# Kernel tuning notes

Measured on AMD Instinct MI355X. Metric: run time of the kernel, lower is better.

Reference implementation:

```python
import jax, jax.numpy as jnp
import numpy as np

MANT_BITS = 8  # static quantize_param_dict values for Positional_0/1/2
_PWL_X = jnp.linspace(-4.0, 4.0, 33, dtype=jnp.float32)
_PWL_Y = 0.5 * _PWL_X * (1.0 + jax.lax.erf(_PWL_X / jnp.sqrt(jnp.float32(2.0))))


def float2fix(x, mantissa_bits):
    """Fixed-point quantization: round to multiples of 2^-mantissa_bits (STE grad)."""
    s = jnp.float32(2.0 ** mantissa_bits)
    q = jnp.round(x * s) / s
    return x + jax.lax.stop_gradient(q - x)


def pwlin_gelu_basic(x, mantissa_bits_in, mantissa_bits_out):
    """Piecewise-linear GELU: quantized input, linear interp of exact GELU on
    [-4,4] (33 breakpoints), 0 for x<-4, identity for x>4, quantized output."""
    xq = float2fix(x, mantissa_bits_in)
    y = jnp.interp(xq, _PWL_X, _PWL_Y)
    y = jnp.where(xq > 4.0, xq, jnp.where(xq < -4.0, jnp.float32(0.0), y))
    return float2fix(y, mantissa_bits_out)


def setup_inputs() -> dict:
    key = jax.random.key(0)
    k_x, k_w1, k_b1, k_w2, k_b2 = jax.random.split(key, 5)
    dim, ff_dim = 1024, 4096
    B, S = 32, 512
    sc1 = 1.0 / np.sqrt(dim)
    sc2 = 1.0 / np.sqrt(ff_dim)
    return {
        "x": jax.random.normal(k_x, (B, S, dim), dtype=jnp.float32),
        "w1": jax.random.uniform(k_w1, (dim, ff_dim), jnp.float32, -sc1, sc1),
        "b1": jax.random.uniform(k_b1, (ff_dim,), jnp.float32, -sc1, sc1),
        "w2": jax.random.uniform(k_w2, (ff_dim, dim), jnp.float32, -sc2, sc2),
        "b2": jax.random.uniform(k_b2, (dim,), jnp.float32, -sc2, sc2),
    }


def reference(x, w1, b1, w2, b2):
    # fc1 GEMM + quantize epilogue
    h = jnp.einsum("bsd,df->bsf", x, w1) + b1          # [B,S,ff_dim]
    h = float2fix(h, MANT_BITS)                         # Positional_0
    # piecewise-linear GELU with quantized in/out
    h = pwlin_gelu_basic(h, MANT_BITS, MANT_BITS)
    h = float2fix(h, MANT_BITS)                         # Positional_1
    # fc2 GEMM + quantize epilogue
    out = jnp.einsum("bsf,fd->bsd", h, w2) + b2         # [B,S,dim]
    return float2fix(out, MANT_BITS)                    # Positional_2
```

## Files before the change

kernel.cpp:

```cpp
#include <hip/hip_runtime.h>
#include <hip/hip_bf16.h>

typedef __bf16 bf16_t;
typedef __bf16 bf16x8 __attribute__((ext_vector_type(8)));
typedef __bf16 bf16x4 __attribute__((ext_vector_type(4)));
typedef float f32x4 __attribute__((ext_vector_type(4)));

#define QS   256.0f
#define QINV 0.00390625f

__device__ __forceinline__ void async_copy16(const bf16_t* g, bf16_t* l) {
  __builtin_amdgcn_global_load_lds(
      (__attribute__((address_space(1))) void*)g,
      (__attribute__((address_space(3))) void*)l,
      16, 0, 0);
}

template <bool GELU, typename OutT>
__global__ __launch_bounds__(256, 4)
void gemm_tile(const bf16_t* __restrict__ A, const bf16_t* __restrict__ Bt,
               const float* __restrict__ bias, OutT* __restrict__ C,
               int M, int N, int K) {
  __shared__ __attribute__((aligned(16))) bf16_t As[128 * 64];
  __shared__ __attribute__((aligned(16))) bf16_t Bs[128 * 64];
  __shared__ float Yt[33];

  const int tid = threadIdx.x;
  const int lane = tid & 63;
  const int wv = tid >> 6;
  const int wy = wv >> 1;
  const int wx = wv & 1;
  const int l15 = lane & 15;
  const int lq = lane >> 4;

  if (GELU && tid < 33) {
    float xv = -4.0f + 0.25f * (float)tid;
    Yt[tid] = 0.5f * xv * (1.0f + erff(xv * 0.70710678f));
  }

  const int mBase = blockIdx.y * 128;
  const int nBase = blockIdx.x * 128;

  const bf16_t* aTile = A + (size_t)mBase * K;
  const bf16_t* bTile = Bt + (size_t)nBase * K;

  f32x4 acc[4][4];
#pragma unroll
  for (int i = 0; i < 4; ++i)
#pragma unroll
    for (int j = 0; j < 4; ++j)
      acc[i][j] = (f32x4){0.f, 0.f, 0.f, 0.f};

  const int srow = tid >> 3;
  const int scb = (((tid & 7) ^ ((tid >> 3) & 7)) * 8);

  const int swz_r = l15 & 7;

  for (int k0 = 0; k0 < K; k0 += 64) {
#pragma unroll
    for (int p = 0; p < 4; ++p) {
      const int row = p * 32 + srow;
      const size_t go = (size_t)row * K + k0 + scb;
      const int lo = (p * 256 + wv * 64) * 8;
      async_copy16(aTile + go, As + lo);
      async_copy16(bTile + go, Bs + lo);
    }
    __syncthreads();

#pragma unroll
    for (int ks = 0; ks < 2; ++ks) {
      const int swzA = ((ks * 4 + lq) ^ swz_r) * 8;
      bf16x8 af[4], bfr[4];
#pragma unroll
      for (int i = 0; i < 4; ++i) {
        af[i]  = *(const bf16x8*)(As + (wy * 64 + i * 16 + l15) * 64 + swzA);
        bfr[i] = *(const bf16x8*)(Bs + (wx * 64 + i * 16 + l15) * 64 + swzA);
      }
#pragma unroll
      for (int i = 0; i < 4; ++i)
#pragma unroll
        for (int j = 0; j < 4; ++j)
          acc[i][j] = __builtin_amdgcn_mfma_f32_16x16x32_bf16(af[i], bfr[j], acc[i][j], 0, 0, 0);
    }
    __syncthreads();
  }

  float bj[4];
#pragma unroll
  for (int j = 0; j < 4; ++j)
    bj[j] = bias[nBase + wx * 64 + j * 16 + l15];

#pragma unroll
  for (int i = 0; i < 4; ++i) {
    const int rb = mBase + wy * 64 + i * 16 + lq * 4;
#pragma unroll
    for (int j = 0; j < 4; ++j) {
      const int cn = nBase + wx * 64 + j * 16 + l15;
#pragma unroll
      for (int r = 0; r < 4; ++r) {
        float c = acc[i][j][r] + bj[j];
        float v;
        if (GELU) {
          float xq = rintf(c * QS) * QINV;
          if (xq > 4.0f) {
            v = xq;
          } else if (xq < -4.0f) {
            v = 0.0f;
          } else {
            float t = (xq + 4.0f) * 4.0f;
            int ii = (int)t;
            ii = ii > 31 ? 31 : ii;
            float f = t - (float)ii;
            float y0 = Yt[ii];
            v = fmaf(f, Yt[ii + 1] - y0, y0);
          }
          v = rintf(v * QS) * QINV;
        } else {
          v = rintf(c * QS) * QINV;
        }
        C[(size_t)(rb + r) * N + cn] = (OutT)v;
      }
    }
  }
}

__global__ void cvt_bf16_kernel(const float* __restrict__ in, bf16_t* __restrict__ out, int n4) {
  int idx = blockIdx.x * blockDim.x + threadIdx.x;
  if (idx < n4) {
    const float4 v = ((const float4*)in)[idx];
    bf16x4 o;
    o[0] = (bf16_t)v.x; o[1] = (bf16_t)v.y; o[2] = (bf16_t)v.z; o[3] = (bf16_t)v.w;
    ((bf16x4*)out)[idx] = o;
  }
}

__global__ void transpose_cvt_kernel(const float* __restrict__ in, bf16_t* __restrict__ out,
                                     int R, int C) {
  __shared__ float t[32][33];
  const int c0 = blockIdx.x * 32;
  const int r0 = blockIdx.y * 32;
  const int tx = threadIdx.x;
  const int ty = threadIdx.y;
#pragma unroll
  for (int dy = 0; dy < 32; dy += 8)
    t[ty + dy][tx] = in[(size_t)(r0 + ty + dy) * C + c0 + tx];
  __syncthreads();
#pragma unroll
  for (int dy = 0; dy < 32; dy += 8)
    out[(size_t)(c0 + ty + dy) * R + r0 + tx] = (bf16_t)t[tx][ty + dy];
}

extern "C" void kernel_launch(void* const* d_in, const int* in_sizes, int n_in,
                              void* d_out, int out_size, void* d_ws, size_t ws_size,
                              hipStream_t stream) {
  const float* x  = (const float*)d_in[0];
  const float* w1 = (const float*)d_in[1];
  const float* b1 = (const float*)d_in[2];
  const float* w2 = (const float*)d_in[3];
  const float* b2 = (const float*)d_in[4];
  float* out = (float*)d_out;

  const int M = 16384, D = 1024, F = 4096;

  char* ws = (char*)d_ws;
  size_t off = 0;
  bf16_t* xb  = (bf16_t*)(ws + off); off += (size_t)M * D * 2;
  bf16_t* w1t = (bf16_t*)(ws + off); off += (size_t)D * F * 2;
  bf16_t* w2t = (bf16_t*)(ws + off); off += (size_t)F * D * 2;
  bf16_t* h   = (bf16_t*)(ws + off);

  cvt_bf16_kernel<<<(M * D / 4 + 255) / 256, 256, 0, stream>>>(x, xb, M * D / 4);
  transpose_cvt_kernel<<<dim3(F / 32, D / 32), dim3(32, 8), 0, stream>>>(w1, w1t, D, F);
  transpose_cvt_kernel<<<dim3(D / 32, F / 32), dim3(32, 8), 0, stream>>>(w2, w2t, F, D);

  gemm_tile<true, bf16_t><<<dim3(F / 128, M / 128), 256, 0, stream>>>(xb, w1t, b1, h, M, F, D);
  gemm_tile<false, float><<<dim3(D / 128, M / 128), 256, 0, stream>>>(h, w2t, b2, out, M, D, F);
}
```

Before: 453.5 us.

## Switch GEMMs to 32x32x16 MFMA and remap fc2 blocks per XCD

Replaces the 4x4 grid of 16x16x32 MFMAs per wave with a 2x2 grid of 32x32x16 MFMAs. This halves the number of LDS fragment loads per k-step and uses the larger-tile instruction, and the epilogue indexing is rewritten to match the 32x32 accumulator layout. It also adds a block-index remap for the fc2 GEMM so that blocks landing on the same XCD share A rows, which should improve L2 reuse. The epilogue stores become less contiguous per lane group, and the remap is hardcoded for an 8x128 grid.

```diff
diff --git a/kernel.cpp b/kernel.cpp
--- a/kernel.cpp
+++ b/kernel.cpp
@@ -4,7 +4,7 @@
 typedef __bf16 bf16_t;
 typedef __bf16 bf16x8 __attribute__((ext_vector_type(8)));
 typedef __bf16 bf16x4 __attribute__((ext_vector_type(4)));
-typedef float f32x4 __attribute__((ext_vector_type(4)));
+typedef float f32x16 __attribute__((ext_vector_type(16)));
 
 #define QS   256.0f
 #define QINV 0.00390625f
@@ -16,7 +16,7 @@
       16, 0, 0);
 }
 
-template <bool GELU, typename OutT>
+template <bool GELU, typename OutT, bool XSWZ>
 __global__ __launch_bounds__(256, 4)
 void gemm_tile(const bf16_t* __restrict__ A, const bf16_t* __restrict__ Bt,
                const float* __restrict__ bias, OutT* __restrict__ C,
@@ -30,31 +30,40 @@
   const int wv = tid >> 6;
   const int wy = wv >> 1;
   const int wx = wv & 1;
-  const int l15 = lane & 15;
-  const int lq = lane >> 4;
+  const int l31 = lane & 31;
+  const int hh = lane >> 5;
 
   if (GELU && tid < 33) {
     float xv = -4.0f + 0.25f * (float)tid;
     Yt[tid] = 0.5f * xv * (1.0f + erff(xv * 0.70710678f));
   }
 
-  const int mBase = blockIdx.y * 128;
-  const int nBase = blockIdx.x * 128;
+  int bx = blockIdx.x, by = blockIdx.y;
+  if (XSWZ) {
+    const int f = by * 8 + bx;
+    const int xcd = f & 7;
+    const int s = f >> 3;
+    bx = s & 7;
+    by = xcd * 16 + (s >> 3);
+  }
+
+  const int mBase = by * 128;
+  const int nBase = bx * 128;
 
   const bf16_t* aTile = A + (size_t)mBase * K;
   const bf16_t* bTile = Bt + (size_t)nBase * K;
 
-  f32x4 acc[4][4];
+  f32x16 acc[2][2];
 #pragma unroll
-  for (int i = 0; i < 4; ++i)
+  for (int i = 0; i < 2; ++i)
 #pragma unroll
-    for (int j = 0; j < 4; ++j)
-      acc[i][j] = (f32x4){0.f, 0.f, 0.f, 0.f};
+    for (int j = 0; j < 2; ++j)
+      acc[i][j] = (f32x16){0.f};
 
   const int srow = tid >> 3;
   const int scb = (((tid & 7) ^ ((tid >> 3) & 7)) * 8);
 
-  const int swz_r = l15 & 7;
+  const int swz_r = l31 & 7;
 
   for (int k0 = 0; k0 < K; k0 += 64) {
 #pragma unroll
@@ -68,37 +77,37 @@
     __syncthreads();
 
 #pragma unroll
-    for (int ks = 0; ks < 2; ++ks) {
-      const int swzA = ((ks * 4 + lq) ^ swz_r) * 8;
-      bf16x8 af[4], bfr[4];
+    for (int ks = 0; ks < 4; ++ks) {
+      const int chunk = ((ks * 2 + hh) ^ swz_r) * 8;
+      bf16x8 af[2], bfr[2];
 #pragma unroll
-      for (int i = 0; i < 4; ++i) {
-        af[i]  = *(const bf16x8*)(As + (wy * 64 + i * 16 + l15) * 64 + swzA);
-        bfr[i] = *(const bf16x8*)(Bs + (wx * 64 + i * 16 + l15) * 64 + swzA);
+      for (int i = 0; i < 2; ++i) {
+        af[i]  = *(const bf16x8*)(As + (wy * 64 + i * 32 + l31) * 64 + chunk);
+        bfr[i] = *(const bf16x8*)(Bs + (wx * 64 + i * 32 + l31) * 64 + chunk);
       }
 #pragma unroll
-      for (int i = 0; i < 4; ++i)
+      for (int i = 0; i < 2; ++i)
 #pragma unroll
-        for (int j = 0; j < 4; ++j)
-          acc[i][j] = __builtin_amdgcn_mfma_f32_16x16x32_bf16(af[i], bfr[j], acc[i][j], 0, 0, 0);
+        for (int j = 0; j < 2; ++j)
+          acc[i][j] = __builtin_amdgcn_mfma_f32_32x32x16_bf16(af[i], bfr[j], acc[i][j], 0, 0, 0);
     }
     __syncthreads();
   }
 
-  float bj[4];
+  float bj[2];
 #pragma unroll
-  for (int j = 0; j < 4; ++j)
-    bj[j] = bias[nBase + wx * 64 + j * 16 + l15];
+  for (int j = 0; j < 2; ++j)
+    bj[j] = bias[nBase + wx * 64 + j * 32 + l31];
 
 #pragma unroll
-  for (int i = 0; i < 4; ++i) {
-    const int rb = mBase + wy * 64 + i * 16 + lq * 4;
+  for (int i = 0; i < 2; ++i) {
 #pragma unroll
-    for (int j = 0; j < 4; ++j) {
-      const int cn = nBase + wx * 64 + j * 16 + l15;
+    for (int j = 0; j < 2; ++j) {
+      const int cn = nBase + wx * 64 + j * 32 + l31;
 #pragma unroll
-      for (int r = 0; r < 4; ++r) {
-        float c = acc[i][j][r] + bj[j];
+      for (int reg = 0; reg < 16; ++reg) {
+        const int rm = mBase + wy * 64 + i * 32 + (reg & 3) + 8 * (reg >> 2) + 4 * hh;
+        float c = acc[i][j][reg] + bj[j];
         float v;
         if (GELU) {
           float xq = rintf(c * QS) * QINV;
@@ -118,7 +127,7 @@
         } else {
           v = rintf(c * QS) * QINV;
         }
-        C[(size_t)(rb + r) * N + cn] = (OutT)v;
+        C[(size_t)rm * N + cn] = (OutT)v;
       }
     }
   }
@@ -173,6 +182,6 @@
   transpose_cvt_kernel<<<dim3(F / 32, D / 32), dim3(32, 8), 0, stream>>>(w1, w1t, D, F);
   transpose_cvt_kernel<<<dim3(D / 32, F / 32), dim3(32, 8), 0, stream>>>(w2, w2t, F, D);
 
-  gemm_tile<true, bf16_t><<<dim3(F / 128, M / 128), 256, 0, stream>>>(xb, w1t, b1, h, M, F, D);
-  gemm_tile<false, float><<<dim3(D / 128, M / 128), 256, 0, stream>>>(h, w2t, b2, out, M, D, F);
+  gemm_tile<true, bf16_t, false><<<dim3(F / 128, M / 128), 256, 0, stream>>>(xb, w1t, b1, h, M, F, D);
+  gemm_tile<false, float, true><<<dim3(D / 128, M / 128), 256, 0, stream>>>(h, w2t, b2, out, M, D, F);
 }
```

After: 460.0 us. Within noise of the previous version (+1.4%).
